# Kernel optimization log

Hardware: AMD Instinct MI355X
Metric: run time of the kernel (lower is better)

The kernel has to match this reference:

```python
import jax, jax.numpy as jnp
import numpy as np

LN_EPS = 1e-5
TOP_K = 2


def setup_inputs() -> dict:
    key = jax.random.key(0)
    ks = jax.random.split(key, 6)
    B, S, D, I, E = 4, 1024, 1024, 4096, 8
    return {
        "hidden_states": jax.random.normal(ks[0], (B, S, D), dtype=jnp.float32),
        "attention_mask": jnp.ones((B, S), dtype=jnp.float32),
        "gate_w": jax.random.normal(ks[1], (E, D), dtype=jnp.float32) * 0.02,
        "w1": jax.random.normal(ks[2], (E, D, I), dtype=jnp.float32) * 0.02,
        "b1": jnp.zeros((E, I), dtype=jnp.float32),
        "w2": jax.random.normal(ks[3], (E, I, D), dtype=jnp.float32) * 0.02,
        "b2": jnp.zeros((E, D), dtype=jnp.float32),
        "ln_gamma": jnp.ones((D,), dtype=jnp.float32),
        "ln_beta": jnp.zeros((D,), dtype=jnp.float32),
    }


def reference(hidden_states, attention_mask, gate_w, w1, b1, w2, b2, ln_gamma, ln_beta):
    B, S, D = hidden_states.shape
    E = gate_w.shape[0]
    h = hidden_states.reshape(-1, D).astype(jnp.float32)  # (T, D)

    # --- gate: softmax over experts, top-2, renormalize ---
    logits = h @ gate_w.T                                  # (T, E)
    probs = jax.nn.softmax(logits, axis=-1)
    rw, sel = jax.lax.top_k(probs, TOP_K)                  # (T, k), (T, k)
    rw = rw / jnp.sum(rw, axis=-1, keepdims=True)

    # per-token dense combine weights: (T, E), zero for non-selected experts
    onehot = jax.nn.one_hot(sel, E, dtype=rw.dtype)        # (T, k, E)
    w_te = jnp.einsum('tk,tke->te', rw, onehot)            # (T, E)

    # --- expert FFNs (dense over all experts; weights zero-out non-selected) ---
    mid = jax.nn.gelu(jnp.einsum('td,edi->eti', h, w1) + b1[:, None, :], approximate=False)
    eout = jnp.einsum('eti,eid->etd', mid, w2) + b2[:, None, :]  # (E, T, D)
    moe_out = jnp.einsum('etd,te->td', eout, w_te)         # (T, D)

    out = moe_out.reshape(B, S, D) * attention_mask[..., None]
    out = hidden_states + out

    # LayerNorm
    mu = jnp.mean(out, axis=-1, keepdims=True)
    var = jnp.var(out, axis=-1, keepdims=True)
    out = (out - mu) * jax.lax.rsqrt(var + LN_EPS) * ln_gamma + ln_beta

    # load balancing loss: mse(expert_usage, uniform)
    T = h.shape[0]
    usage = jnp.sum(onehot, axis=(0, 1)) / T               # (E,)
    aux_loss = jnp.mean((usage - 1.0 / E) ** 2)
    return out, aux_loss
```

## Files before the change

### kernel.cpp

```cpp
#include <hip/hip_runtime.h>
#include <hip/hip_bf16.h>
#include <math.h>

#define T_TOK 4096
#define D_DIM 1024
#define I_DIM 4096
#define E_EXP 8
#define MAX_TILES 72

typedef __attribute__((ext_vector_type(8))) short bf16x8;
typedef __attribute__((ext_vector_type(4))) float f32x4;

__device__ __forceinline__ unsigned short f2bf(float x) {
    unsigned int u = __float_as_uint(x);
    u += 0x7fffu + ((u >> 16) & 1u);
    return (unsigned short)(u >> 16);
}

__device__ __forceinline__ void glds16(const unsigned short* g, unsigned short* l) {
    __builtin_amdgcn_global_load_lds(
        (const __attribute__((address_space(1))) unsigned int*)g,
        (__attribute__((address_space(3))) unsigned int*)(unsigned int)(unsigned long long)(void*)l,
        16, 0, 0);
}

__global__ void gate_kernel(const float* __restrict__ h, const float* __restrict__ gw,
                            int* __restrict__ counts, int* __restrict__ sel,
                            float* __restrict__ wgt) {
    int t = blockIdx.x;
    int tid = threadIdx.x;
    float acc[E_EXP];
#pragma unroll
    for (int e = 0; e < E_EXP; e++) acc[e] = 0.f;
    const float* hr = h + (size_t)t * D_DIM;
    for (int d = tid; d < D_DIM; d += 256) {
        float hv = hr[d];
#pragma unroll
        for (int e = 0; e < E_EXP; e++) acc[e] += hv * gw[e * D_DIM + d];
    }
#pragma unroll
    for (int e = 0; e < E_EXP; e++)
        for (int off = 32; off > 0; off >>= 1) acc[e] += __shfl_down(acc[e], off, 64);
    __shared__ float red[4][E_EXP];
    int wave = tid >> 6, lane = tid & 63;
    if (lane == 0) {
#pragma unroll
        for (int e = 0; e < E_EXP; e++) red[wave][e] = acc[e];
    }
    __syncthreads();
    if (tid == 0) {
        float lg[E_EXP];
#pragma unroll
        for (int e = 0; e < E_EXP; e++) lg[e] = red[0][e] + red[1][e] + red[2][e] + red[3][e];
        float mx = lg[0];
#pragma unroll
        for (int e = 1; e < E_EXP; e++) mx = fmaxf(mx, lg[e]);
        float p[E_EXP];
#pragma unroll
        for (int e = 0; e < E_EXP; e++) p[e] = expf(lg[e] - mx);
        int i0 = 0; float b0 = p[0];
#pragma unroll
        for (int e = 1; e < E_EXP; e++) if (p[e] > b0) { b0 = p[e]; i0 = e; }
        int i1 = -1; float b1v = -1.f;
#pragma unroll
        for (int e = 0; e < E_EXP; e++) if (e != i0 && p[e] > b1v) { b1v = p[e]; i1 = e; }
        float den = b0 + b1v;
        sel[2 * t] = i0; sel[2 * t + 1] = i1;
        wgt[2 * t] = b0 / den; wgt[2 * t + 1] = b1v / den;
        atomicAdd(&counts[i0], 1);
        atomicAdd(&counts[i1], 1);
    }
}

__global__ void offsets_kernel(const int* __restrict__ counts, int* __restrict__ offs,
                               int* __restrict__ cursors, float* __restrict__ aux_out,
                               int* __restrict__ tile_e, int* __restrict__ tile_m,
                               int* __restrict__ ntiles) {
    if (blockIdx.x == 0 && threadIdx.x == 0) {
        int off = 0; float aux = 0.f; int nt = 0;
        for (int e = 0; e < E_EXP; e++) {
            offs[e] = off; off += counts[e]; cursors[e] = 0;
            float u = (float)counts[e] / (float)T_TOK;
            float d = u - 1.0f / (float)E_EXP;
            aux += d * d;
            for (int m0 = 0; m0 < counts[e]; m0 += 128) {
                tile_e[nt] = e; tile_m[nt] = m0; nt++;
            }
        }
        ntiles[0] = nt;
        aux_out[0] = aux / (float)E_EXP;
    }
}

__global__ void scatter_kernel(const int* __restrict__ sel, const float* __restrict__ wgt,
                               const int* __restrict__ offs, int* __restrict__ cursors,
                               int* __restrict__ tok_list, float* __restrict__ tok_w,
                               int* __restrict__ slot_of) {
    int t = blockIdx.x * 256 + threadIdx.x;
    if (t >= T_TOK) return;
#pragma unroll
    for (int k = 0; k < 2; k++) {
        int e = sel[2 * t + k];
        int pos = atomicAdd(&cursors[e], 1);
        int idx = offs[e] + pos;
        tok_list[idx] = t;
        tok_w[idx] = wgt[2 * t + k];
        slot_of[2 * t + k] = idx;
    }
}

__global__ void cvtH_kernel(const float* __restrict__ src, unsigned short* __restrict__ dst) {
    size_t i = ((size_t)blockIdx.x * 256 + threadIdx.x) * 8;
    float4 a = *(const float4*)(src + i);
    float4 b = *(const float4*)(src + i + 4);
    union { unsigned short u[8]; uint4 v; } o;
    o.u[0] = f2bf(a.x); o.u[1] = f2bf(a.y); o.u[2] = f2bf(a.z); o.u[3] = f2bf(a.w);
    o.u[4] = f2bf(b.x); o.u[5] = f2bf(b.y); o.u[6] = f2bf(b.z); o.u[7] = f2bf(b.w);
    *(uint4*)(dst + i) = o.v;
}

__global__ void transpose_cvt_kernel(const float* __restrict__ src, unsigned short* __restrict__ dst,
                                     int R, int C) {
    __shared__ float tile[32][33];
    int e = blockIdx.z;
    const float* s = src + (size_t)e * R * C;
    unsigned short* d = dst + (size_t)e * R * C;
    int c0 = blockIdx.x * 32, r0 = blockIdx.y * 32;
    int tx = threadIdx.x, ty = threadIdx.y;
#pragma unroll
    for (int j = 0; j < 4; j++)
        tile[ty + 8 * j][tx] = s[(size_t)(r0 + ty + 8 * j) * C + c0 + tx];
    __syncthreads();
#pragma unroll
    for (int j = 0; j < 4; j++)
        d[(size_t)(c0 + ty + 8 * j) * R + r0 + tx] = f2bf(tile[tx][ty + 8 * j]);
}

template <int MODE>
__launch_bounds__(256)
__global__ void moe_gemm_kernel(const unsigned short* __restrict__ Abase,
                                const unsigned short* __restrict__ Bt,
                                const float* __restrict__ bias,
                                const int* __restrict__ counts, const int* __restrict__ offs,
                                const int* __restrict__ tile_e, const int* __restrict__ tile_m,
                                const int* __restrict__ ntiles,
                                const int* __restrict__ tok_list, const float* __restrict__ tok_w,
                                unsigned short* __restrict__ midout, float* __restrict__ slotbuf) {
    constexpr int K = (MODE == 0) ? D_DIM : I_DIM;
    constexpr int N = (MODE == 0) ? I_DIM : D_DIM;
    const int tix = blockIdx.x;
    if (tix >= ntiles[0]) return;
    const int e = tile_e[tix];
    const int m0 = tile_m[tix];
    const int Ne = counts[e];
    const int n0 = blockIdx.y * 128;
    const int seg = offs[e];

    __shared__ __align__(16) unsigned short lA[128 * 32];
    __shared__ __align__(16) unsigned short lB[128 * 32];

    const int tid = threadIdx.x;
    const int lane = tid & 63;
    const int wave = tid >> 6;
    const int wm = (wave >> 1) * 64;
    const int wn = (wave & 1) * 64;
    const int quad = lane >> 4;
    const int l15 = lane & 15;

    const int srow = wave * 32 + (lane >> 2);
    const int scol = (lane & 3) * 8;

    const unsigned short *pA0, *pA1;
    {
        int mr0 = m0 + srow, mr1 = mr0 + 16;
        size_t arow0, arow1;
        if (MODE == 0) {
            arow0 = (size_t)tok_list[seg + (mr0 < Ne ? mr0 : 0)] * K;
            arow1 = (size_t)tok_list[seg + (mr1 < Ne ? mr1 : 0)] * K;
        } else {
            arow0 = (size_t)(seg + (mr0 < Ne ? mr0 : 0)) * K;
            arow1 = (size_t)(seg + (mr1 < Ne ? mr1 : 0)) * K;
        }
        pA0 = Abase + arow0 + scol;
        pA1 = Abase + arow1 + scol;
    }
    const unsigned short* Bte = Bt + (size_t)e * N * K;
    const unsigned short* pB0 = Bte + (size_t)(n0 + srow) * K + scol;
    const unsigned short* pB1 = Bte + (size_t)(n0 + srow + 16) * K + scol;

    unsigned short* dA0 = lA + (wave * 32) * 32;
    unsigned short* dA1 = lA + (wave * 32 + 16) * 32;
    unsigned short* dB0 = lB + (wave * 32) * 32;
    unsigned short* dB1 = lB + (wave * 32 + 16) * 32;

    f32x4 acc[4][4];
#pragma unroll
    for (int i = 0; i < 4; i++)
#pragma unroll
        for (int j = 0; j < 4; j++) acc[i][j] = (f32x4){0.f, 0.f, 0.f, 0.f};

    for (int k0 = 0; k0 < K; k0 += 32) {
        glds16(pA0, dA0);
        glds16(pA1, dA1);
        glds16(pB0, dB0);
        glds16(pB1, dB1);
        pA0 += 32; pA1 += 32; pB0 += 32; pB1 += 32;
        __syncthreads();
        bf16x8 af[4], bfr[4];
#pragma unroll
        for (int i = 0; i < 4; i++)
            af[i] = *(const bf16x8*)&lA[(wm + i * 16 + l15) * 32 + quad * 8];
#pragma unroll
        for (int j = 0; j < 4; j++)
            bfr[j] = *(const bf16x8*)&lB[(wn + j * 16 + l15) * 32 + quad * 8];
#pragma unroll
        for (int i = 0; i < 4; i++)
#pragma unroll
            for (int j = 0; j < 4; j++)
                acc[i][j] = __builtin_amdgcn_mfma_f32_16x16x32_bf16(af[i], bfr[j], acc[i][j], 0, 0, 0);
        __syncthreads();
    }

    const float* be = bias + (size_t)e * N;
#pragma unroll
    for (int i = 0; i < 4; i++) {
        int mbase = m0 + wm + i * 16 + quad * 4;
#pragma unroll
        for (int j = 0; j < 4; j++) {
            int n = n0 + wn + j * 16 + l15;
            float bv = be[n];
#pragma unroll
            for (int r = 0; r < 4; r++) {
                int m = mbase + r;
                if (m < Ne) {
                    float v = acc[i][j][r] + bv;
                    if (MODE == 0) {
                        v = 0.5f * v * (1.0f + erff(v * 0.70710678118654752f));
                        midout[(size_t)(seg + m) * N + n] = f2bf(v);
                    } else {
                        slotbuf[(size_t)(seg + m) * N + n] = tok_w[seg + m] * v;
                    }
                }
            }
        }
    }
}

__global__ void ln_kernel(const float* __restrict__ hs, const float* __restrict__ mask,
                          const float* __restrict__ slotbuf, const int* __restrict__ slot_of,
                          const float* __restrict__ gamma, const float* __restrict__ beta,
                          float* __restrict__ outp) {
    int t = blockIdx.x, tid = threadIdx.x;
    int s0 = slot_of[2 * t], s1 = slot_of[2 * t + 1];
    float mk = mask[t];
    const float4* hr = (const float4*)(hs + (size_t)t * D_DIM);
    const float4* p0 = (const float4*)(slotbuf + (size_t)s0 * D_DIM);
    const float4* p1 = (const float4*)(slotbuf + (size_t)s1 * D_DIM);
    float4 hv = hr[tid], a = p0[tid], b = p1[tid];
    float x0 = hv.x + mk * (a.x + b.x);
    float x1 = hv.y + mk * (a.y + b.y);
    float x2 = hv.z + mk * (a.z + b.z);
    float x3 = hv.w + mk * (a.w + b.w);
    float sum = x0 + x1 + x2 + x3;
    float sq = x0 * x0 + x1 * x1 + x2 * x2 + x3 * x3;
    for (int off = 32; off > 0; off >>= 1) {
        sum += __shfl_down(sum, off, 64);
        sq += __shfl_down(sq, off, 64);
    }
    __shared__ float rsum[4], rsq[4];
    __shared__ float mu_s, rstd_s;
    int wave = tid >> 6, lane = tid & 63;
    if (lane == 0) { rsum[wave] = sum; rsq[wave] = sq; }
    __syncthreads();
    if (tid == 0) {
        float s = rsum[0] + rsum[1] + rsum[2] + rsum[3];
        float q = rsq[0] + rsq[1] + rsq[2] + rsq[3];
        float mu = s / (float)D_DIM;
        float var = q / (float)D_DIM - mu * mu;
        mu_s = mu; rstd_s = rsqrtf(var + 1e-5f);
    }
    __syncthreads();
    float mu = mu_s, rstd = rstd_s;
    const float4* g4 = (const float4*)gamma;
    const float4* b4 = (const float4*)beta;
    float4 g = g4[tid], bb = b4[tid];
    float4 o;
    o.x = (x0 - mu) * rstd * g.x + bb.x;
    o.y = (x1 - mu) * rstd * g.y + bb.y;
    o.z = (x2 - mu) * rstd * g.z + bb.z;
    o.w = (x3 - mu) * rstd * g.w + bb.w;
    ((float4*)(outp + (size_t)t * D_DIM))[tid] = o;
}

extern "C" void kernel_launch(void* const* d_in, const int* in_sizes, int n_in,
                              void* d_out, int out_size, void* d_ws, size_t ws_size,
                              hipStream_t stream) {
    const float* hs    = (const float*)d_in[0];
    const float* mask  = (const float*)d_in[1];
    const float* gw    = (const float*)d_in[2];
    const float* w1    = (const float*)d_in[3];
    const float* b1    = (const float*)d_in[4];
    const float* w2    = (const float*)d_in[5];
    const float* b2    = (const float*)d_in[6];
    const float* gamma = (const float*)d_in[7];
    const float* beta  = (const float*)d_in[8];
    float* out = (float*)d_out;

    char* ws = (char*)d_ws;
    int*   counts   = (int*)(ws + 0);
    int*   cursors  = (int*)(ws + 64);
    int*   offs     = (int*)(ws + 128);
    int*   ntiles   = (int*)(ws + 256);
    int*   tile_e   = (int*)(ws + 512);
    int*   tile_m   = (int*)(ws + 1024);
    int*   sel      = (int*)(ws + 4096);
    float* wgt      = (float*)(ws + 4096 + 1 * 32768);
    int*   slot_of  = (int*)(ws + 4096 + 2 * 32768);
    int*   tok_list = (int*)(ws + 4096 + 3 * 32768);
    float* tok_w    = (float*)(ws + 4096 + 4 * 32768);
    unsigned short* Hbf = (unsigned short*)(ws + (1ull << 20));
    unsigned short* W1t = (unsigned short*)(ws + (9ull << 20));
    unsigned short* W2t = (unsigned short*)(ws + (73ull << 20));
    unsigned short* mid = (unsigned short*)(ws + (137ull << 20));
    float* slotbuf      = (float*)(ws + (201ull << 20));

    hipMemsetAsync(counts, 0, 64, stream);
    gate_kernel<<<T_TOK, 256, 0, stream>>>(hs, gw, counts, sel, wgt);
    offsets_kernel<<<1, 64, 0, stream>>>(counts, offs, cursors, out + (size_t)T_TOK * D_DIM,
                                         tile_e, tile_m, ntiles);
    scatter_kernel<<<T_TOK / 256, 256, 0, stream>>>(sel, wgt, offs, cursors, tok_list, tok_w, slot_of);
    cvtH_kernel<<<(T_TOK * D_DIM / 8) / 256, 256, 0, stream>>>(hs, Hbf);
    transpose_cvt_kernel<<<dim3(I_DIM / 32, D_DIM / 32, E_EXP), dim3(32, 8), 0, stream>>>(w1, W1t, D_DIM, I_DIM);
    transpose_cvt_kernel<<<dim3(D_DIM / 32, I_DIM / 32, E_EXP), dim3(32, 8), 0, stream>>>(w2, W2t, I_DIM, D_DIM);
    moe_gemm_kernel<0><<<dim3(MAX_TILES, I_DIM / 128), 256, 0, stream>>>(
        Hbf, W1t, b1, counts, offs, tile_e, tile_m, ntiles, tok_list, tok_w, mid, nullptr);
    moe_gemm_kernel<1><<<dim3(MAX_TILES, D_DIM / 128), 256, 0, stream>>>(
        mid, W2t, b2, counts, offs, tile_e, tile_m, ntiles, tok_list, tok_w, nullptr, slotbuf);
    ln_kernel<<<T_TOK, 256, 0, stream>>>(hs, mask, slotbuf, slot_of, gamma, beta, out);
}
```

Baseline: 770.9 us.

## Enlarge MoE GEMM tiles with 4-stage async LDS pipeline and XCD-aware block remap

The grouped expert GEMMs move to 256-row M tiles, 256 or 128 column N tiles and 512-thread blocks with 8 waves. Global-to-LDS loads run through a 4-buffer ring, using explicit vmcnt waits and one barrier per k-step instead of two syncthreads. Block indices are remapped so neighbouring tiles land on the same XCD, and MFMA sections get raised priority. The aim is better data reuse and load latency hiding, at the cost of larger tiles that waste more padding on small experts and heavier LDS and register use.

```diff
diff --git a/kernel.cpp b/kernel.cpp
--- a/kernel.cpp
+++ b/kernel.cpp
@@ -6,7 +6,7 @@
 #define D_DIM 1024
 #define I_DIM 4096
 #define E_EXP 8
-#define MAX_TILES 72
+#define MAX_TILES 48
 
 typedef __attribute__((ext_vector_type(8))) short bf16x8;
 typedef __attribute__((ext_vector_type(4))) float f32x4;
@@ -22,6 +22,16 @@
         (const __attribute__((address_space(1))) unsigned int*)g,
         (__attribute__((address_space(3))) unsigned int*)(unsigned int)(unsigned long long)(void*)l,
         16, 0, 0);
+}
+
+#define VMWAIT4 asm volatile("s_waitcnt vmcnt(4)" ::: "memory")
+#define VMWAIT3 asm volatile("s_waitcnt vmcnt(3)" ::: "memory")
+#define VMWAIT0 asm volatile("s_waitcnt vmcnt(0)" ::: "memory")
+
+__device__ __forceinline__ void bar() {
+    asm volatile("" ::: "memory");
+    __builtin_amdgcn_s_barrier();
+    asm volatile("" ::: "memory");
 }
 
 __global__ void gate_kernel(const float* __restrict__ h, const float* __restrict__ gw,
@@ -83,7 +93,7 @@
             float u = (float)counts[e] / (float)T_TOK;
             float d = u - 1.0f / (float)E_EXP;
             aux += d * d;
-            for (int m0 = 0; m0 < counts[e]; m0 += 128) {
+            for (int m0 = 0; m0 < counts[e]; m0 += 256) {
                 tile_e[nt] = e; tile_m[nt] = m0; nt++;
             }
         }
@@ -137,7 +147,7 @@
 }
 
 template <int MODE>
-__launch_bounds__(256)
+__launch_bounds__(512, 2)
 __global__ void moe_gemm_kernel(const unsigned short* __restrict__ Abase,
                                 const unsigned short* __restrict__ Bt,
                                 const float* __restrict__ bias,
@@ -146,94 +156,130 @@
                                 const int* __restrict__ ntiles,
                                 const int* __restrict__ tok_list, const float* __restrict__ tok_w,
                                 unsigned short* __restrict__ midout, float* __restrict__ slotbuf) {
-    constexpr int K = (MODE == 0) ? D_DIM : I_DIM;
-    constexpr int N = (MODE == 0) ? I_DIM : D_DIM;
-    const int tix = blockIdx.x;
+    constexpr int K  = (MODE == 0) ? D_DIM : I_DIM;
+    constexpr int N  = (MODE == 0) ? I_DIM : D_DIM;
+    constexpr int BN = (MODE == 0) ? 256 : 128;
+    constexpr int NJ = BN / 64;
+    constexpr int SB = BN / 128;
+    constexpr int NT = K / 32;
+
+    __shared__ __align__(16) unsigned short lA[4][256 * 32];
+    __shared__ __align__(16) unsigned short lB[4][BN * 32];
+
+    const int nwg  = gridDim.x * gridDim.y;
+    const int flat = blockIdx.y * gridDim.x + blockIdx.x;
+    const int q8 = nwg >> 3, r8 = nwg & 7;
+    const int xcd = flat & 7, pos = flat >> 3;
+    const int id2 = (xcd < r8 ? xcd * (q8 + 1) : r8 * (q8 + 1) + (xcd - r8) * q8) + pos;
+    const int tix = id2 / gridDim.y;
+    const int nb  = id2 % gridDim.y;
     if (tix >= ntiles[0]) return;
-    const int e = tile_e[tix];
-    const int m0 = tile_m[tix];
-    const int Ne = counts[e];
-    const int n0 = blockIdx.y * 128;
+
+    const int e   = tile_e[tix];
+    const int m0  = tile_m[tix];
+    const int Ne  = counts[e];
     const int seg = offs[e];
-
-    __shared__ __align__(16) unsigned short lA[128 * 32];
-    __shared__ __align__(16) unsigned short lB[128 * 32];
-
-    const int tid = threadIdx.x;
+    const int n0  = nb * BN;
+
+    const int tid  = threadIdx.x;
+    const int w    = tid >> 6;
     const int lane = tid & 63;
-    const int wave = tid >> 6;
-    const int wm = (wave >> 1) * 64;
-    const int wn = (wave & 1) * 64;
     const int quad = lane >> 4;
-    const int l15 = lane & 15;
-
-    const int srow = wave * 32 + (lane >> 2);
-    const int scol = (lane & 3) * 8;
-
-    const unsigned short *pA0, *pA1;
+    const int l15  = lane & 15;
+    const int wm   = (w >> 2) * 128;
+    const int wn   = (w & 3) * (NJ * 16);
+
+    const int lrow = lane >> 2;
+    const int lcol = (lane & 3) * 8;
+    const unsigned short* gA0;
+    const unsigned short* gA1;
     {
-        int mr0 = m0 + srow, mr1 = mr0 + 16;
-        size_t arow0, arow1;
-        if (MODE == 0) {
-            arow0 = (size_t)tok_list[seg + (mr0 < Ne ? mr0 : 0)] * K;
-            arow1 = (size_t)tok_list[seg + (mr1 < Ne ? mr1 : 0)] * K;
+        int mr0 = m0 + w * 32 + lrow;
+        int mr1 = mr0 + 16;
+        int c0 = (mr0 < Ne) ? mr0 : 0;
+        int c1 = (mr1 < Ne) ? mr1 : 0;
+        size_t r0, r1;
+        if (MODE == 0) { r0 = (size_t)tok_list[seg + c0] * K; r1 = (size_t)tok_list[seg + c1] * K; }
+        else           { r0 = (size_t)(seg + c0) * K;         r1 = (size_t)(seg + c1) * K; }
+        gA0 = Abase + r0 + lcol;
+        gA1 = Abase + r1 + lcol;
+    }
+    const unsigned short* Bte = Bt + (size_t)e * N * K;
+    const unsigned short* gB0 = Bte + (size_t)(n0 + w * (16 * SB) + lrow) * K + lcol;
+    const unsigned short* gB1 = gB0 + (size_t)16 * K;
+
+    auto ISSUE = [&](int kt2) {
+        const int b2  = kt2 & 3;
+        const int off = kt2 * 32;
+        glds16(gA0 + off, &lA[b2][w * 1024]);
+        glds16(gA1 + off, &lA[b2][w * 1024 + 512]);
+        glds16(gB0 + off, &lB[b2][w * (SB * 512)]);
+        if constexpr (MODE == 0) glds16(gB1 + off, &lB[b2][w * 1024 + 512]);
+    };
+
+    f32x4 acc[8][NJ];
+#pragma unroll
+    for (int a = 0; a < 8; a++)
+#pragma unroll
+        for (int j = 0; j < NJ; j++) acc[a][j] = (f32x4){0.f, 0.f, 0.f, 0.f};
+
+    const int sc = quad * 8;
+
+    auto TILE = [&](int kt2) {
+        const unsigned short* LA = lA[kt2 & 3];
+        const unsigned short* LB = lB[kt2 & 3];
+        bf16x8 bv[NJ];
+#pragma unroll
+        for (int j = 0; j < NJ; j++)
+            bv[j] = *(const bf16x8*)&LB[(wn + j * 16 + l15) * 32 + sc];
+#pragma unroll
+        for (int pm = 0; pm < 2; pm++) {
+            bf16x8 av[4];
+#pragma unroll
+            for (int ii = 0; ii < 4; ii++)
+                av[ii] = *(const bf16x8*)&LA[(wm + pm * 64 + ii * 16 + l15) * 32 + sc];
+            __builtin_amdgcn_s_setprio(1);
+#pragma unroll
+            for (int ii = 0; ii < 4; ii++)
+#pragma unroll
+                for (int j = 0; j < NJ; j++)
+                    acc[pm * 4 + ii][j] = __builtin_amdgcn_mfma_f32_16x16x32_bf16(
+                        av[ii], bv[j], acc[pm * 4 + ii][j], 0, 0, 0);
+            __builtin_amdgcn_s_setprio(0);
+        }
+    };
+
+    ISSUE(0);
+    ISSUE(1);
+
+    for (int kt = 0; kt < NT; kt += 2) {
+        if constexpr (MODE == 0) { VMWAIT4; } else { VMWAIT3; }
+        bar();
+        if (kt + 2 < NT) ISSUE(kt + 2);
+        TILE(kt);
+        if (kt + 3 < NT) {
+            if constexpr (MODE == 0) { VMWAIT4; } else { VMWAIT3; }
         } else {
-            arow0 = (size_t)(seg + (mr0 < Ne ? mr0 : 0)) * K;
-            arow1 = (size_t)(seg + (mr1 < Ne ? mr1 : 0)) * K;
+            VMWAIT0;
         }
-        pA0 = Abase + arow0 + scol;
-        pA1 = Abase + arow1 + scol;
-    }
-    const unsigned short* Bte = Bt + (size_t)e * N * K;
-    const unsigned short* pB0 = Bte + (size_t)(n0 + srow) * K + scol;
-    const unsigned short* pB1 = Bte + (size_t)(n0 + srow + 16) * K + scol;
-
-    unsigned short* dA0 = lA + (wave * 32) * 32;
-    unsigned short* dA1 = lA + (wave * 32 + 16) * 32;
-    unsigned short* dB0 = lB + (wave * 32) * 32;
-    unsigned short* dB1 = lB + (wave * 32 + 16) * 32;
-
-    f32x4 acc[4][4];
-#pragma unroll
-    for (int i = 0; i < 4; i++)
-#pragma unroll
-        for (int j = 0; j < 4; j++) acc[i][j] = (f32x4){0.f, 0.f, 0.f, 0.f};
-
-    for (int k0 = 0; k0 < K; k0 += 32) {
-        glds16(pA0, dA0);
-        glds16(pA1, dA1);
-        glds16(pB0, dB0);
-        glds16(pB1, dB1);
-        pA0 += 32; pA1 += 32; pB0 += 32; pB1 += 32;
-        __syncthreads();
-        bf16x8 af[4], bfr[4];
-#pragma unroll
-        for (int i = 0; i < 4; i++)
-            af[i] = *(const bf16x8*)&lA[(wm + i * 16 + l15) * 32 + quad * 8];
-#pragma unroll
-        for (int j = 0; j < 4; j++)
-            bfr[j] = *(const bf16x8*)&lB[(wn + j * 16 + l15) * 32 + quad * 8];
-#pragma unroll
-        for (int i = 0; i < 4; i++)
-#pragma unroll
-            for (int j = 0; j < 4; j++)
-                acc[i][j] = __builtin_amdgcn_mfma_f32_16x16x32_bf16(af[i], bfr[j], acc[i][j], 0, 0, 0);
-        __syncthreads();
+        bar();
+        if (kt + 3 < NT) ISSUE(kt + 3);
+        TILE(kt + 1);
     }
 
     const float* be = bias + (size_t)e * N;
 #pragma unroll
-    for (int i = 0; i < 4; i++) {
-        int mbase = m0 + wm + i * 16 + quad * 4;
-#pragma unroll
-        for (int j = 0; j < 4; j++) {
-            int n = n0 + wn + j * 16 + l15;
-            float bv = be[n];
+    for (int a = 0; a < 8; a++) {
+        const int mbase = m0 + wm + (a >> 2) * 64 + (a & 3) * 16 + quad * 4;
+#pragma unroll
+        for (int j = 0; j < NJ; j++) {
+            const int n = n0 + wn + j * 16 + l15;
+            const float bvl = be[n];
 #pragma unroll
             for (int r = 0; r < 4; r++) {
-                int m = mbase + r;
+                const int m = mbase + r;
                 if (m < Ne) {
-                    float v = acc[i][j][r] + bv;
+                    float v = acc[a][j][r] + bvl;
                     if (MODE == 0) {
                         v = 0.5f * v * (1.0f + erff(v * 0.70710678118654752f));
                         midout[(size_t)(seg + m) * N + n] = f2bf(v);
@@ -332,9 +378,9 @@
     cvtH_kernel<<<(T_TOK * D_DIM / 8) / 256, 256, 0, stream>>>(hs, Hbf);
     transpose_cvt_kernel<<<dim3(I_DIM / 32, D_DIM / 32, E_EXP), dim3(32, 8), 0, stream>>>(w1, W1t, D_DIM, I_DIM);
     transpose_cvt_kernel<<<dim3(D_DIM / 32, I_DIM / 32, E_EXP), dim3(32, 8), 0, stream>>>(w2, W2t, I_DIM, D_DIM);
-    moe_gemm_kernel<0><<<dim3(MAX_TILES, I_DIM / 128), 256, 0, stream>>>(
+    moe_gemm_kernel<0><<<dim3(MAX_TILES, I_DIM / 256), 512, 0, stream>>>(
         Hbf, W1t, b1, counts, offs, tile_e, tile_m, ntiles, tok_list, tok_w, mid, nullptr);
-    moe_gemm_kernel<1><<<dim3(MAX_TILES, D_DIM / 128), 256, 0, stream>>>(
+    moe_gemm_kernel<1><<<dim3(MAX_TILES, D_DIM / 128), 512, 0, stream>>>(
         mid, W2t, b2, counts, offs, tile_e, tile_m, ntiles, tok_list, tok_w, nullptr, slotbuf);
     ln_kernel<<<T_TOK, 256, 0, stream>>>(hs, mask, slotbuf, slot_of, gamma, beta, out);
 }
```

Result: slower. 817.4 us (+6.0%).
